# Kernel optimization log

Hardware: AMD Instinct MI355X
Metric: run time of the kernel (lower is better)

The kernel has to match this reference:

```python
import jax, jax.numpy as jnp
import numpy as np

VOCAB = 32000
EMBED = 512
NUM_CLASS = 5
LEAVES = 8192
N_NODES = 2 * LEAVES - 1


def _build_tree(n_leaves):
    """Balanced binary tree over n_leaves leaves, nodes listed in post-order
    (children always appear before their parent), matching the recursive
    traversal order of the original torch module."""
    is_leaf, word, left, right = [], [], [], []

    def rec(lo, hi):
        if hi - lo == 1:
            is_leaf.append(1)
            word.append((lo * 2654435761) % VOCAB)
            left.append(0)
            right.append(0)
        else:
            mid = (lo + hi) // 2
            l = rec(lo, mid)
            r = rec(mid, hi)
            is_leaf.append(0)
            word.append(0)
            left.append(l)
            right.append(r)
        return len(is_leaf) - 1

    rec(0, n_leaves)
    return (np.asarray(is_leaf, np.int32), np.asarray(word, np.int32),
            np.asarray(left, np.int32), np.asarray(right, np.int32))


def setup_inputs() -> dict:
    key = jax.random.key(0)
    k1, k2, k3, k4, k5 = jax.random.split(key, 5)
    is_leaf, word, left, right = _build_tree(LEAVES)
    scale = 0.05
    return {
        "is_leaf": jnp.asarray(is_leaf),
        "word": jnp.asarray(word),
        "left": jnp.asarray(left),
        "right": jnp.asarray(right),
        "emb": jax.random.normal(k1, (VOCAB, EMBED), jnp.float32) * scale,
        "W": jax.random.normal(k2, (EMBED, 2 * EMBED), jnp.float32) * scale,
        "bW": jax.random.normal(k3, (EMBED,), jnp.float32) * scale,
        "P": jax.random.normal(k4, (NUM_CLASS, EMBED), jnp.float32) * scale,
        "bP": jax.random.normal(k5, (NUM_CLASS,), jnp.float32) * scale,
    }


def reference(is_leaf, word, left, right, emb, W, bW, P, bP):
    n = is_leaf.shape[0]

    def step(H, xs):
        idx, lf, wd, li, ri = xs
        # internal node: relu(W @ [h_left; h_right] + b)
        pair = jnp.concatenate([H[li], H[ri]])          # [2D]
        internal = pair @ W.T + bW                       # [D]
        leaf = emb[wd]                                   # [D]
        h = jax.nn.relu(jnp.where(lf == 1, leaf, internal))
        return H.at[idx].set(h), None

    H0 = jnp.zeros((n, EMBED), emb.dtype)
    xs = (jnp.arange(n, dtype=jnp.int32), is_leaf, word, left, right)
    H, _ = jax.lax.scan(step, H0, xs)
    # per-node class logits, rows in traversal (post-)order: [N, num_class]
    return H @ P.T + bP
```

## Files before the change

### kernel.cpp

```cpp
#include <hip/hip_runtime.h>


#define EMBED 512
#define K2    1024
#define WOFF  (EMBED * K2)

typedef _Float16 half8 __attribute__((ext_vector_type(8)));
typedef float    floatx4 __attribute__((ext_vector_type(4)));

__device__ __forceinline__ float relu_f(float x) { return fmaxf(x, 0.0f); }

#define GLDS16(gp, lp)                                                        \
    __builtin_amdgcn_global_load_lds(                                         \
        (const __attribute__((address_space(1))) void*)(gp),                  \
        (__attribute__((address_space(3))) void*)(lp), 16, 0, 0)

__global__ __launch_bounds__(256)
void pack_w(const float* __restrict__ W,
            _Float16* __restrict__ Whp, _Float16* __restrict__ Wlp)
{
    int t = blockIdx.x * 256 + threadIdx.x;
    int n = t >> 7, kc = t & 127;
    const float* src = W + (size_t)n * K2 + kc * 8;
    int s = kc >> 2, quad = kc & 3;
    int lane = (quad << 4) | (n & 15);
    size_t off = (size_t)(n >> 4) * 16384 + (size_t)s * 512 + (size_t)lane * 8;
    half8 hi, lo;
#pragma unroll
    for (int j = 0; j < 8; ++j) {
        float w = src[j];
        _Float16 h = (_Float16)w;
        hi[j] = h;
        lo[j] = (_Float16)(w - (float)h);
    }
    *(half8*)(Whp + off) = hi;
    *(half8*)(Wlp + off) = lo;
}

__global__ __launch_bounds__(256)
void leaf_kernel(const float* __restrict__ emb, const int* __restrict__ word,
                 _Float16* __restrict__ Hh, _Float16* __restrict__ Hl, int nLeaves)
{
    int t = blockIdx.x * 256 + threadIdx.x;
    int m = t >> 6, lane = t & 63;
    if (m >= nLeaves) return;
    int idx = 2 * m - __popc(m);
    int wd = word[idx];
    const float4* src = (const float4*)(emb + (size_t)wd * EMBED) + lane * 2;
    float4 a = src[0], b = src[1];
    float v[8] = {a.x, a.y, a.z, a.w, b.x, b.y, b.z, b.w};
    half8 hi, lo;
#pragma unroll
    for (int j = 0; j < 8; ++j) {
        float x = relu_f(v[j]);
        _Float16 h = (_Float16)x;
        hi[j] = h;
        lo[j] = (_Float16)(x - (float)h);
    }
    *(half8*)(Hh + (size_t)idx * EMBED + lane * 8) = hi;
    *(half8*)(Hl + (size_t)idx * EMBED + lane * 8) = lo;
}

__global__ __launch_bounds__(256)
void gemm_big(const _Float16* H,
              const _Float16* __restrict__ Wp,
              const float* __restrict__ bW,
              _Float16* Hh, _Float16* Hl,
              int h, int M, int hoff)
{
    __shared__ _Float16 lds[48 * 512];

    int tid = threadIdx.x;
    int wave = tid >> 6, lane = tid & 63;
    int q = lane >> 4, r = lane & 15;
    int wm = wave >> 1, wn = wave & 1;
    int bm0 = blockIdx.x * 64, bn0 = blockIdx.y * 128;

    int ms = bm0 + wave * 16 + r;
    if (ms >= M) ms = M - 1;
    int node_s = ((ms + 1) << (h + 1)) - 2 - __popc(ms);
    int aL = (node_s - (1 << h)) * EMBED + q * 8;
    int aR = (node_s - 1) * EMBED + q * 8;

    floatx4 acc[2][4];
#pragma unroll
    for (int i = 0; i < 2; ++i)
#pragma unroll
        for (int j = 0; j < 4; ++j) acc[i][j] = (floatx4){0.f, 0.f, 0.f, 0.f};

    for (int kc = 0; kc < 16; ++kc) {
        int abase = (kc < 8) ? (aL + kc * 64) : (aR + (kc - 8) * 64);
#pragma unroll
        for (int i = 0; i < 4; ++i) {
            int s2 = i >> 1, hl = i & 1;
            const _Float16* gp = H + abase + s2 * 32 + (hl ? hoff : 0);
            GLDS16(gp, &lds[(wave * 4 + i) * 512]);
        }
#pragma unroll
        for (int j = 0; j < 8; ++j) {
            int u = wave * 2 + (j >> 2), s2 = (j >> 1) & 1, hl = j & 1;
            const _Float16* gp = Wp + (size_t)(blockIdx.y * 8 + u) * 16384
                               + (kc * 2 + s2) * 512 + (hl ? WOFF : 0) + lane * 8;
            GLDS16(gp, &lds[8192 + (wave * 8 + j) * 512]);
        }
        __syncthreads();

#pragma unroll
        for (int s2 = 0; s2 < 2; ++s2) {
            half8 ah[2], al[2], bh[4], bl[4];
#pragma unroll
            for (int t2 = 0; t2 < 2; ++t2) {
                int t = wm * 2 + t2;
                ah[t2] = *(const half8*)&lds[((t * 2 + s2) * 2 + 0) * 512 + lane * 8];
                al[t2] = *(const half8*)&lds[((t * 2 + s2) * 2 + 1) * 512 + lane * 8];
            }
#pragma unroll
            for (int u2 = 0; u2 < 4; ++u2) {
                int u = wn * 4 + u2;
                bh[u2] = *(const half8*)&lds[8192 + ((u * 2 + s2) * 2 + 0) * 512 + lane * 8];
                bl[u2] = *(const half8*)&lds[8192 + ((u * 2 + s2) * 2 + 1) * 512 + lane * 8];
            }
#pragma unroll
            for (int t2 = 0; t2 < 2; ++t2)
#pragma unroll
                for (int u2 = 0; u2 < 4; ++u2) {
                    acc[t2][u2] = __builtin_amdgcn_mfma_f32_16x16x32_f16(ah[t2], bh[u2], acc[t2][u2], 0, 0, 0);
                    acc[t2][u2] = __builtin_amdgcn_mfma_f32_16x16x32_f16(ah[t2], bl[u2], acc[t2][u2], 0, 0, 0);
                    acc[t2][u2] = __builtin_amdgcn_mfma_f32_16x16x32_f16(al[t2], bh[u2], acc[t2][u2], 0, 0, 0);
                }
        }
        __syncthreads();
    }

#pragma unroll
    for (int t2 = 0; t2 < 2; ++t2)
#pragma unroll
        for (int reg = 0; reg < 4; ++reg) {
            int m = bm0 + (wm * 2 + t2) * 16 + q * 4 + reg;
            if (m < M) {
                int node = ((m + 1) << (h + 1)) - 2 - __popc(m);
#pragma unroll
                for (int u2 = 0; u2 < 4; ++u2) {
                    int col = bn0 + (wn * 4 + u2) * 16 + r;
                    float v = relu_f(acc[t2][u2][reg] + bW[col]);
                    _Float16 hi = (_Float16)v;
                    Hh[(size_t)node * EMBED + col] = hi;
                    Hl[(size_t)node * EMBED + col] = (_Float16)(v - (float)hi);
                }
            }
        }
}

__global__ __launch_bounds__(256)
void gemm_splitk(const _Float16* __restrict__ Hh, const _Float16* __restrict__ Hl,
                 const _Float16* __restrict__ Wp,
                 const float* __restrict__ bW,
                 _Float16* HhO, _Float16* HlO,
                 int h, int M)
{
    __shared__ float red[4 * 256];

    int tid = threadIdx.x;
    int wave = tid >> 6, lane = tid & 63;
    int q = lane >> 4, r = lane & 15;
    int mt = blockIdx.x, u = blockIdx.y;

    int m = mt * 16 + r;
    if (m >= M) m = M - 1;
    int idx = ((m + 1) << (h + 1)) - 2 - __popc(m);
    int childRow = (wave < 2) ? (idx - (1 << h)) : (idx - 1);
    int kbase = (wave & 1) * 256;
    const _Float16* pAh = Hh + (size_t)childRow * EMBED + kbase + q * 8;
    const _Float16* pAl = Hl + (size_t)childRow * EMBED + kbase + q * 8;
    const _Float16* pB  = Wp + (size_t)u * 16384 + (size_t)(wave * 8) * 512 + lane * 8;

    floatx4 acc = (floatx4){0.f, 0.f, 0.f, 0.f};
#pragma unroll
    for (int s = 0; s < 8; ++s) {
        half8 ah = *(const half8*)(pAh + s * 32);
        half8 al = *(const half8*)(pAl + s * 32);
        half8 bh = *(const half8*)(pB + s * 512);
        half8 bl = *(const half8*)(pB + s * 512 + WOFF);
        acc = __builtin_amdgcn_mfma_f32_16x16x32_f16(ah, bh, acc, 0, 0, 0);
        acc = __builtin_amdgcn_mfma_f32_16x16x32_f16(ah, bl, acc, 0, 0, 0);
        acc = __builtin_amdgcn_mfma_f32_16x16x32_f16(al, bh, acc, 0, 0, 0);
    }
#pragma unroll
    for (int reg = 0; reg < 4; ++reg)
        red[wave * 256 + (q * 4 + reg) * 16 + r] = acc[reg];
    __syncthreads();

    int row = tid >> 4, col = tid & 15;
    float v = red[row * 16 + col] + red[256 + row * 16 + col]
            + red[512 + row * 16 + col] + red[768 + row * 16 + col];
    int mm = mt * 16 + row;
    if (mm < M) {
        int node = ((mm + 1) << (h + 1)) - 2 - __popc(mm);
        int colg = u * 16 + col;
        float x = relu_f(v + bW[colg]);
        _Float16 hi = (_Float16)x;
        HhO[(size_t)node * EMBED + colg] = hi;
        HlO[(size_t)node * EMBED + colg] = (_Float16)(x - (float)hi);
    }
}

__global__ __launch_bounds__(256)
void out_kernel(const _Float16* __restrict__ Hh, const _Float16* __restrict__ Hl,
                const float* __restrict__ P, const float* __restrict__ bP,
                float* __restrict__ out, int nNodes)
{
    int t = blockIdx.x * 256 + threadIdx.x;
    int node = t >> 6, lane = t & 63;
    if (node >= nNodes) return;
    half8 hv = *(const half8*)(Hh + (size_t)node * EMBED + lane * 8);
    half8 lv = *(const half8*)(Hl + (size_t)node * EMBED + lane * 8);
    float hx[8];
#pragma unroll
    for (int j = 0; j < 8; ++j) hx[j] = (float)hv[j] + (float)lv[j];
    float s[5];
#pragma unroll
    for (int c = 0; c < 5; ++c) {
        const float* p = P + c * EMBED + lane * 8;
        float4 p0 = *(const float4*)p;
        float4 p1 = *(const float4*)(p + 4);
        s[c] = hx[0] * p0.x + hx[1] * p0.y + hx[2] * p0.z + hx[3] * p0.w
             + hx[4] * p1.x + hx[5] * p1.y + hx[6] * p1.z + hx[7] * p1.w;
    }
#pragma unroll
    for (int o = 32; o > 0; o >>= 1)
#pragma unroll
        for (int c = 0; c < 5; ++c)
            s[c] += __shfl_down(s[c], o, 64);
    if (lane == 0) {
#pragma unroll
        for (int c = 0; c < 5; ++c)
            out[(size_t)node * 5 + c] = s[c] + bP[c];
    }
}

extern "C" void kernel_launch(void* const* d_in, const int* in_sizes, int n_in,
                              void* d_out, int out_size, void* d_ws, size_t ws_size,
                              hipStream_t stream)
{
    const int*   word = (const int*)d_in[1];
    const float* emb  = (const float*)d_in[4];
    const float* W    = (const float*)d_in[5];
    const float* bW   = (const float*)d_in[6];
    const float* P    = (const float*)d_in[7];
    const float* bP   = (const float*)d_in[8];
    float* out = (float*)d_out;

    int nNodes  = in_sizes[0];
    int nLeaves = (nNodes + 1) / 2;
    int L = 0;
    while ((1 << L) < nLeaves) ++L;

    int hoff = (nNodes + 1) * EMBED;
    _Float16* Hh  = (_Float16*)d_ws;
    _Float16* Hl  = Hh + hoff;
    _Float16* Whp = Hl + hoff;

    pack_w<<<dim3(256), dim3(256), 0, stream>>>(W, Whp, Whp + WOFF);
    leaf_kernel<<<dim3((nLeaves * 64 + 255) / 256), dim3(256), 0, stream>>>(
        emb, word, Hh, Hl, nLeaves);
    for (int h = 1; h <= L; ++h) {
        int M = 1 << (L - h);
        if (M >= 512) {
            gemm_big<<<dim3(M / 64, 4), dim3(256), 0, stream>>>(
                Hh, Whp, bW, Hh, Hl, h, M, hoff);
        } else {
            gemm_splitk<<<dim3((M + 15) / 16, 32), dim3(256), 0, stream>>>(
                Hh, Hl, Whp, bW, Hh, Hl, h, M);
        }
    }
    out_kernel<<<dim3((nNodes * 64 + 255) / 256), dim3(256), 0, stream>>>(
        Hh, Hl, P, bP, out, nNodes);
}
```

Baseline: 284.0 us.

## Fuse all tree levels into one persistent kernel with grid barriers

Replaces the sequence of per-level kernel launches (pack, leaf, 13 GEMM levels, output) with a single persistent 256-block kernel that separates the phases with atomic-counter grid barriers. The aim is to remove launch overhead and inter-kernel gaps, which are significant here because the upper tree levels carry very little work. The risks are that all 256 blocks must be co-resident for the spin barriers to make progress, that spin-waiting has its own cost, and that level count and block count are now hard-coded constants. The barrier also gives up after a spin limit instead of waiting indefinitely.

```diff
diff --git a/kernel.cpp b/kernel.cpp
--- a/kernel.cpp
+++ b/kernel.cpp
@@ -4,6 +4,8 @@
 #define EMBED 512
 #define K2    1024
 #define WOFF  (EMBED * K2)
+#define NBLK  256
+#define LVL   13
 
 typedef _Float16 half8 __attribute__((ext_vector_type(8)));
 typedef float    floatx4 __attribute__((ext_vector_type(4)));
@@ -15,226 +17,246 @@
         (const __attribute__((address_space(1))) void*)(gp),                  \
         (__attribute__((address_space(3))) void*)(lp), 16, 0, 0)
 
-__global__ __launch_bounds__(256)
-void pack_w(const float* __restrict__ W,
-            _Float16* __restrict__ Whp, _Float16* __restrict__ Wlp)
+__device__ __forceinline__ void gsync(int* cnt, int idx)
 {
-    int t = blockIdx.x * 256 + threadIdx.x;
-    int n = t >> 7, kc = t & 127;
-    const float* src = W + (size_t)n * K2 + kc * 8;
-    int s = kc >> 2, quad = kc & 3;
-    int lane = (quad << 4) | (n & 15);
-    size_t off = (size_t)(n >> 4) * 16384 + (size_t)s * 512 + (size_t)lane * 8;
-    half8 hi, lo;
-#pragma unroll
-    for (int j = 0; j < 8; ++j) {
-        float w = src[j];
-        _Float16 h = (_Float16)w;
-        hi[j] = h;
-        lo[j] = (_Float16)(w - (float)h);
-    }
-    *(half8*)(Whp + off) = hi;
-    *(half8*)(Wlp + off) = lo;
+    __syncthreads();
+    if (threadIdx.x == 0) {
+        __threadfence();
+        __hip_atomic_fetch_add(&cnt[idx], 1, __ATOMIC_RELEASE,
+                               __HIP_MEMORY_SCOPE_AGENT);
+        int spins = 0;
+        while (__hip_atomic_load(&cnt[idx], __ATOMIC_ACQUIRE,
+                                 __HIP_MEMORY_SCOPE_AGENT) < NBLK) {
+            __builtin_amdgcn_s_sleep(2);
+            if (++spins > (1 << 22)) break;
+        }
+        __threadfence();
+    }
+    __syncthreads();
 }
 
-__global__ __launch_bounds__(256)
-void leaf_kernel(const float* __restrict__ emb, const int* __restrict__ word,
-                 _Float16* __restrict__ Hh, _Float16* __restrict__ Hl, int nLeaves)
-{
-    int t = blockIdx.x * 256 + threadIdx.x;
-    int m = t >> 6, lane = t & 63;
-    if (m >= nLeaves) return;
-    int idx = 2 * m - __popc(m);
-    int wd = word[idx];
-    const float4* src = (const float4*)(emb + (size_t)wd * EMBED) + lane * 2;
-    float4 a = src[0], b = src[1];
-    float v[8] = {a.x, a.y, a.z, a.w, b.x, b.y, b.z, b.w};
-    half8 hi, lo;
-#pragma unroll
-    for (int j = 0; j < 8; ++j) {
-        float x = relu_f(v[j]);
-        _Float16 h = (_Float16)x;
-        hi[j] = h;
-        lo[j] = (_Float16)(x - (float)h);
-    }
-    *(half8*)(Hh + (size_t)idx * EMBED + lane * 8) = hi;
-    *(half8*)(Hl + (size_t)idx * EMBED + lane * 8) = lo;
-}
-
-__global__ __launch_bounds__(256)
-void gemm_big(const _Float16* H,
-              const _Float16* __restrict__ Wp,
-              const float* __restrict__ bW,
-              _Float16* Hh, _Float16* Hl,
-              int h, int M, int hoff)
+__global__ __launch_bounds__(256, 1)
+void mega(const int* __restrict__ word, const float* __restrict__ emb,
+          const float* __restrict__ W, const float* __restrict__ bW,
+          const float* __restrict__ P, const float* __restrict__ bP,
+          _Float16* Hh, _Float16* Hl,
+          _Float16* Whp,
+          int* cnt, float* out, int nNodes, int nLeaves, int hoff)
 {
     __shared__ _Float16 lds[48 * 512];
+    float* red = (float*)lds;
 
     int tid = threadIdx.x;
     int wave = tid >> 6, lane = tid & 63;
     int q = lane >> 4, r = lane & 15;
     int wm = wave >> 1, wn = wave & 1;
-    int bm0 = blockIdx.x * 64, bn0 = blockIdx.y * 128;
-
-    int ms = bm0 + wave * 16 + r;
-    if (ms >= M) ms = M - 1;
-    int node_s = ((ms + 1) << (h + 1)) - 2 - __popc(ms);
-    int aL = (node_s - (1 << h)) * EMBED + q * 8;
-    int aR = (node_s - 1) * EMBED + q * 8;
-
-    floatx4 acc[2][4];
-#pragma unroll
-    for (int i = 0; i < 2; ++i)
-#pragma unroll
-        for (int j = 0; j < 4; ++j) acc[i][j] = (floatx4){0.f, 0.f, 0.f, 0.f};
-
-    for (int kc = 0; kc < 16; ++kc) {
-        int abase = (kc < 8) ? (aL + kc * 64) : (aR + (kc - 8) * 64);
-#pragma unroll
-        for (int i = 0; i < 4; ++i) {
-            int s2 = i >> 1, hl = i & 1;
-            const _Float16* gp = H + abase + s2 * 32 + (hl ? hoff : 0);
-            GLDS16(gp, &lds[(wave * 4 + i) * 512]);
-        }
+
+    {
+        int t = blockIdx.x * 256 + tid;
+        int n = t >> 7, kc = t & 127;
+        const float* src = W + (size_t)n * K2 + kc * 8;
+        int s = kc >> 2, quad = kc & 3;
+        int ln = (quad << 4) | (n & 15);
+        size_t off = (size_t)(n >> 4) * 16384 + (size_t)s * 512 + (size_t)ln * 8;
+        half8 hi, lo;
 #pragma unroll
         for (int j = 0; j < 8; ++j) {
-            int u = wave * 2 + (j >> 2), s2 = (j >> 1) & 1, hl = j & 1;
-            const _Float16* gp = Wp + (size_t)(blockIdx.y * 8 + u) * 16384
-                               + (kc * 2 + s2) * 512 + (hl ? WOFF : 0) + lane * 8;
-            GLDS16(gp, &lds[8192 + (wave * 8 + j) * 512]);
-        }
-        __syncthreads();
-
-#pragma unroll
-        for (int s2 = 0; s2 < 2; ++s2) {
-            half8 ah[2], al[2], bh[4], bl[4];
-#pragma unroll
-            for (int t2 = 0; t2 < 2; ++t2) {
-                int t = wm * 2 + t2;
-                ah[t2] = *(const half8*)&lds[((t * 2 + s2) * 2 + 0) * 512 + lane * 8];
-                al[t2] = *(const half8*)&lds[((t * 2 + s2) * 2 + 1) * 512 + lane * 8];
-            }
-#pragma unroll
-            for (int u2 = 0; u2 < 4; ++u2) {
-                int u = wn * 4 + u2;
-                bh[u2] = *(const half8*)&lds[8192 + ((u * 2 + s2) * 2 + 0) * 512 + lane * 8];
-                bl[u2] = *(const half8*)&lds[8192 + ((u * 2 + s2) * 2 + 1) * 512 + lane * 8];
-            }
+            float w = src[j];
+            _Float16 h16 = (_Float16)w;
+            hi[j] = h16;
+            lo[j] = (_Float16)(w - (float)h16);
+        }
+        *(half8*)(Whp + off) = hi;
+        *(half8*)(Whp + WOFF + off) = lo;
+    }
+    {
+#pragma unroll
+        for (int i = 0; i < 8; ++i) {
+            int m = blockIdx.x * 32 + wave * 8 + i;
+            if (m < nLeaves) {
+                int idx = 2 * m - __popc(m);
+                int wd = word[idx];
+                const float4* src = (const float4*)(emb + (size_t)wd * EMBED) + lane * 2;
+                float4 a = src[0], b = src[1];
+                float v[8] = {a.x, a.y, a.z, a.w, b.x, b.y, b.z, b.w};
+                half8 hi, lo;
+#pragma unroll
+                for (int j = 0; j < 8; ++j) {
+                    float x = relu_f(v[j]);
+                    _Float16 h16 = (_Float16)x;
+                    hi[j] = h16;
+                    lo[j] = (_Float16)(x - (float)h16);
+                }
+                *(half8*)(Hh + (size_t)idx * EMBED + lane * 8) = hi;
+                *(half8*)(Hl + (size_t)idx * EMBED + lane * 8) = lo;
+            }
+        }
+    }
+    gsync(cnt, 0);
+
+    for (int h = 1; h <= 4; ++h) {
+        int M = 1 << (LVL - h);
+        int mtiles = M >> 6;
+        int jobs = mtiles * 4;
+        if ((int)blockIdx.x < jobs) {
+            int bx = blockIdx.x % mtiles, by = blockIdx.x / mtiles;
+            int bm0 = bx * 64, bn0 = by * 128;
+
+            int ms = bm0 + wave * 16 + r;
+            if (ms >= M) ms = M - 1;
+            int node_s = ((ms + 1) << (h + 1)) - 2 - __popc(ms);
+            int aL = (node_s - (1 << h)) * EMBED + q * 8;
+            int aR = (node_s - 1) * EMBED + q * 8;
+
+            floatx4 acc[2][4];
+#pragma unroll
+            for (int i = 0; i < 2; ++i)
+#pragma unroll
+                for (int j = 0; j < 4; ++j) acc[i][j] = (floatx4){0.f, 0.f, 0.f, 0.f};
+
+            for (int kc = 0; kc < 16; ++kc) {
+                int abase = (kc < 8) ? (aL + kc * 64) : (aR + (kc - 8) * 64);
+#pragma unroll
+                for (int i = 0; i < 4; ++i) {
+                    int s2 = i >> 1, hl = i & 1;
+                    const _Float16* gp = Hh + abase + s2 * 32 + (hl ? hoff : 0);
+                    GLDS16(gp, &lds[(wave * 4 + i) * 512]);
+                }
+#pragma unroll
+                for (int j = 0; j < 8; ++j) {
+                    int u = wave * 2 + (j >> 2), s2 = (j >> 1) & 1, hl = j & 1;
+                    const _Float16* gp = Whp + (size_t)(by * 8 + u) * 16384
+                                       + (kc * 2 + s2) * 512 + (hl ? WOFF : 0) + lane * 8;
+                    GLDS16(gp, &lds[8192 + (wave * 8 + j) * 512]);
+                }
+                __syncthreads();
+
+#pragma unroll
+                for (int s2 = 0; s2 < 2; ++s2) {
+                    half8 ah[2], al[2], bh[4], bl[4];
+#pragma unroll
+                    for (int t2 = 0; t2 < 2; ++t2) {
+                        int t = wm * 2 + t2;
+                        ah[t2] = *(const half8*)&lds[((t * 2 + s2) * 2 + 0) * 512 + lane * 8];
+                        al[t2] = *(const half8*)&lds[((t * 2 + s2) * 2 + 1) * 512 + lane * 8];
+                    }
+#pragma unroll
+                    for (int u2 = 0; u2 < 4; ++u2) {
+                        int u = wn * 4 + u2;
+                        bh[u2] = *(const half8*)&lds[8192 + ((u * 2 + s2) * 2 + 0) * 512 + lane * 8];
+                        bl[u2] = *(const half8*)&lds[8192 + ((u * 2 + s2) * 2 + 1) * 512 + lane * 8];
+                    }
+#pragma unroll
+                    for (int t2 = 0; t2 < 2; ++t2)
+#pragma unroll
+                        for (int u2 = 0; u2 < 4; ++u2) {
+                            acc[t2][u2] = __builtin_amdgcn_mfma_f32_16x16x32_f16(ah[t2], bh[u2], acc[t2][u2], 0, 0, 0);
+                            acc[t2][u2] = __builtin_amdgcn_mfma_f32_16x16x32_f16(ah[t2], bl[u2], acc[t2][u2], 0, 0, 0);
+                            acc[t2][u2] = __builtin_amdgcn_mfma_f32_16x16x32_f16(al[t2], bh[u2], acc[t2][u2], 0, 0, 0);
+                        }
+                }
+                __syncthreads();
+            }
+
 #pragma unroll
             for (int t2 = 0; t2 < 2; ++t2)
 #pragma unroll
-                for (int u2 = 0; u2 < 4; ++u2) {
-                    acc[t2][u2] = __builtin_amdgcn_mfma_f32_16x16x32_f16(ah[t2], bh[u2], acc[t2][u2], 0, 0, 0);
-                    acc[t2][u2] = __builtin_amdgcn_mfma_f32_16x16x32_f16(ah[t2], bl[u2], acc[t2][u2], 0, 0, 0);
-                    acc[t2][u2] = __builtin_amdgcn_mfma_f32_16x16x32_f16(al[t2], bh[u2], acc[t2][u2], 0, 0, 0);
-                }
-        }
-        __syncthreads();
-    }
-
-#pragma unroll
-    for (int t2 = 0; t2 < 2; ++t2)
-#pragma unroll
-        for (int reg = 0; reg < 4; ++reg) {
-            int m = bm0 + (wm * 2 + t2) * 16 + q * 4 + reg;
-            if (m < M) {
-                int node = ((m + 1) << (h + 1)) - 2 - __popc(m);
-#pragma unroll
-                for (int u2 = 0; u2 < 4; ++u2) {
-                    int col = bn0 + (wn * 4 + u2) * 16 + r;
-                    float v = relu_f(acc[t2][u2][reg] + bW[col]);
-                    _Float16 hi = (_Float16)v;
-                    Hh[(size_t)node * EMBED + col] = hi;
-                    Hl[(size_t)node * EMBED + col] = (_Float16)(v - (float)hi);
-                }
-            }
-        }
-}
-
-__global__ __launch_bounds__(256)
-void gemm_splitk(const _Float16* __restrict__ Hh, const _Float16* __restrict__ Hl,
-                 const _Float16* __restrict__ Wp,
-                 const float* __restrict__ bW,
-                 _Float16* HhO, _Float16* HlO,
-                 int h, int M)
-{
-    __shared__ float red[4 * 256];
-
-    int tid = threadIdx.x;
-    int wave = tid >> 6, lane = tid & 63;
-    int q = lane >> 4, r = lane & 15;
-    int mt = blockIdx.x, u = blockIdx.y;
-
-    int m = mt * 16 + r;
-    if (m >= M) m = M - 1;
-    int idx = ((m + 1) << (h + 1)) - 2 - __popc(m);
-    int childRow = (wave < 2) ? (idx - (1 << h)) : (idx - 1);
-    int kbase = (wave & 1) * 256;
-    const _Float16* pAh = Hh + (size_t)childRow * EMBED + kbase + q * 8;
-    const _Float16* pAl = Hl + (size_t)childRow * EMBED + kbase + q * 8;
-    const _Float16* pB  = Wp + (size_t)u * 16384 + (size_t)(wave * 8) * 512 + lane * 8;
-
-    floatx4 acc = (floatx4){0.f, 0.f, 0.f, 0.f};
-#pragma unroll
-    for (int s = 0; s < 8; ++s) {
-        half8 ah = *(const half8*)(pAh + s * 32);
-        half8 al = *(const half8*)(pAl + s * 32);
-        half8 bh = *(const half8*)(pB + s * 512);
-        half8 bl = *(const half8*)(pB + s * 512 + WOFF);
-        acc = __builtin_amdgcn_mfma_f32_16x16x32_f16(ah, bh, acc, 0, 0, 0);
-        acc = __builtin_amdgcn_mfma_f32_16x16x32_f16(ah, bl, acc, 0, 0, 0);
-        acc = __builtin_amdgcn_mfma_f32_16x16x32_f16(al, bh, acc, 0, 0, 0);
-    }
-#pragma unroll
-    for (int reg = 0; reg < 4; ++reg)
-        red[wave * 256 + (q * 4 + reg) * 16 + r] = acc[reg];
-    __syncthreads();
-
-    int row = tid >> 4, col = tid & 15;
-    float v = red[row * 16 + col] + red[256 + row * 16 + col]
-            + red[512 + row * 16 + col] + red[768 + row * 16 + col];
-    int mm = mt * 16 + row;
-    if (mm < M) {
-        int node = ((mm + 1) << (h + 1)) - 2 - __popc(mm);
-        int colg = u * 16 + col;
-        float x = relu_f(v + bW[colg]);
-        _Float16 hi = (_Float16)x;
-        HhO[(size_t)node * EMBED + colg] = hi;
-        HlO[(size_t)node * EMBED + colg] = (_Float16)(x - (float)hi);
-    }
-}
-
-__global__ __launch_bounds__(256)
-void out_kernel(const _Float16* __restrict__ Hh, const _Float16* __restrict__ Hl,
-                const float* __restrict__ P, const float* __restrict__ bP,
-                float* __restrict__ out, int nNodes)
-{
-    int t = blockIdx.x * 256 + threadIdx.x;
-    int node = t >> 6, lane = t & 63;
-    if (node >= nNodes) return;
-    half8 hv = *(const half8*)(Hh + (size_t)node * EMBED + lane * 8);
-    half8 lv = *(const half8*)(Hl + (size_t)node * EMBED + lane * 8);
-    float hx[8];
-#pragma unroll
-    for (int j = 0; j < 8; ++j) hx[j] = (float)hv[j] + (float)lv[j];
-    float s[5];
-#pragma unroll
-    for (int c = 0; c < 5; ++c) {
-        const float* p = P + c * EMBED + lane * 8;
-        float4 p0 = *(const float4*)p;
-        float4 p1 = *(const float4*)(p + 4);
-        s[c] = hx[0] * p0.x + hx[1] * p0.y + hx[2] * p0.z + hx[3] * p0.w
-             + hx[4] * p1.x + hx[5] * p1.y + hx[6] * p1.z + hx[7] * p1.w;
-    }
-#pragma unroll
-    for (int o = 32; o > 0; o >>= 1)
-#pragma unroll
-        for (int c = 0; c < 5; ++c)
-            s[c] += __shfl_down(s[c], o, 64);
-    if (lane == 0) {
-#pragma unroll
-        for (int c = 0; c < 5; ++c)
-            out[(size_t)node * 5 + c] = s[c] + bP[c];
+                for (int reg = 0; reg < 4; ++reg) {
+                    int m = bm0 + (wm * 2 + t2) * 16 + q * 4 + reg;
+                    if (m < M) {
+                        int node = ((m + 1) << (h + 1)) - 2 - __popc(m);
+#pragma unroll
+                        for (int u2 = 0; u2 < 4; ++u2) {
+                            int col = bn0 + (wn * 4 + u2) * 16 + r;
+                            float v = relu_f(acc[t2][u2][reg] + bW[col]);
+                            _Float16 hi = (_Float16)v;
+                            Hh[(size_t)node * EMBED + col] = hi;
+                            Hl[(size_t)node * EMBED + col] = (_Float16)(v - (float)hi);
+                        }
+                    }
+                }
+        }
+        gsync(cnt, h);
+    }
+
+    for (int h = 5; h <= LVL; ++h) {
+        int M = 1 << (LVL - h);
+        int jm = (M + 15) >> 4;
+        int jobs = jm * 32;
+        for (int job = blockIdx.x; job < jobs; job += NBLK) {
+            int mt = job % jm, u = job / jm;
+
+            int m = mt * 16 + r;
+            if (m >= M) m = M - 1;
+            int idx = ((m + 1) << (h + 1)) - 2 - __popc(m);
+            int childRow = (wave < 2) ? (idx - (1 << h)) : (idx - 1);
+            int kbase = (wave & 1) * 256;
+            const _Float16* pAh = Hh + (size_t)childRow * EMBED + kbase + q * 8;
+            const _Float16* pAl = Hl + (size_t)childRow * EMBED + kbase + q * 8;
+            const _Float16* pB  = Whp + (size_t)u * 16384 + (size_t)(wave * 8) * 512 + lane * 8;
+
+            floatx4 acc = (floatx4){0.f, 0.f, 0.f, 0.f};
+#pragma unroll
+            for (int s = 0; s < 8; ++s) {
+                half8 ah = *(const half8*)(pAh + s * 32);
+                half8 al = *(const half8*)(pAl + s * 32);
+                half8 bh = *(const half8*)(pB + s * 512);
+                half8 bl = *(const half8*)(pB + s * 512 + WOFF);
+                acc = __builtin_amdgcn_mfma_f32_16x16x32_f16(ah, bh, acc, 0, 0, 0);
+                acc = __builtin_amdgcn_mfma_f32_16x16x32_f16(ah, bl, acc, 0, 0, 0);
+                acc = __builtin_amdgcn_mfma_f32_16x16x32_f16(al, bh, acc, 0, 0, 0);
+            }
+#pragma unroll
+            for (int reg = 0; reg < 4; ++reg)
+                red[wave * 256 + (q * 4 + reg) * 16 + r] = acc[reg];
+            __syncthreads();
+
+            int row = tid >> 4, col = tid & 15;
+            float v = red[row * 16 + col] + red[256 + row * 16 + col]
+                    + red[512 + row * 16 + col] + red[768 + row * 16 + col];
+            int mm = mt * 16 + row;
+            if (mm < M) {
+                int node = ((mm + 1) << (h + 1)) - 2 - __popc(mm);
+                int colg = u * 16 + col;
+                float x = relu_f(v + bW[colg]);
+                _Float16 hi = (_Float16)x;
+                Hh[(size_t)node * EMBED + colg] = hi;
+                Hl[(size_t)node * EMBED + colg] = (_Float16)(x - (float)hi);
+            }
+            __syncthreads();
+        }
+        gsync(cnt, h);
+    }
+
+#pragma unroll
+    for (int i = 0; i < 16; ++i) {
+        int node = blockIdx.x * 64 + wave * 16 + i;
+        if (node < nNodes) {
+            half8 hv = *(const half8*)(Hh + (size_t)node * EMBED + lane * 8);
+            half8 lv = *(const half8*)(Hl + (size_t)node * EMBED + lane * 8);
+            float hx[8];
+#pragma unroll
+            for (int j = 0; j < 8; ++j) hx[j] = (float)hv[j] + (float)lv[j];
+            float s[5];
+#pragma unroll
+            for (int c = 0; c < 5; ++c) {
+                const float* p = P + c * EMBED + lane * 8;
+                float4 p0 = *(const float4*)p;
+                float4 p1 = *(const float4*)(p + 4);
+                s[c] = hx[0] * p0.x + hx[1] * p0.y + hx[2] * p0.z + hx[3] * p0.w
+                     + hx[4] * p1.x + hx[5] * p1.y + hx[6] * p1.z + hx[7] * p1.w;
+            }
+#pragma unroll
+            for (int o = 32; o > 0; o >>= 1)
+#pragma unroll
+                for (int c = 0; c < 5; ++c)
+                    s[c] += __shfl_down(s[c], o, 64);
+            if (lane == 0) {
+#pragma unroll
+                for (int c = 0; c < 5; ++c)
+                    out[(size_t)node * 5 + c] = s[c] + bP[c];
+            }
+        }
     }
 }
 
@@ -252,27 +274,14 @@
 
     int nNodes  = in_sizes[0];
     int nLeaves = (nNodes + 1) / 2;
-    int L = 0;
-    while ((1 << L) < nLeaves) ++L;
 
     int hoff = (nNodes + 1) * EMBED;
     _Float16* Hh  = (_Float16*)d_ws;
     _Float16* Hl  = Hh + hoff;
     _Float16* Whp = Hl + hoff;
-
-    pack_w<<<dim3(256), dim3(256), 0, stream>>>(W, Whp, Whp + WOFF);
-    leaf_kernel<<<dim3((nLeaves * 64 + 255) / 256), dim3(256), 0, stream>>>(
-        emb, word, Hh, Hl, nLeaves);
-    for (int h = 1; h <= L; ++h) {
-        int M = 1 << (L - h);
-        if (M >= 512) {
-            gemm_big<<<dim3(M / 64, 4), dim3(256), 0, stream>>>(
-                Hh, Whp, bW, Hh, Hl, h, M, hoff);
-        } else {
-            gemm_splitk<<<dim3((M + 15) / 16, 32), dim3(256), 0, stream>>>(
-                Hh, Hl, Whp, bW, Hh, Hl, h, M);
-        }
-    }
-    out_kernel<<<dim3((nNodes * 64 + 255) / 256), dim3(256), 0, stream>>>(
-        Hh, Hl, P, bP, out, nNodes);
+    int* cnt = (int*)(Whp + 2 * WOFF);
+
+    hipMemsetAsync(cnt, 0, 64, stream);
+    mega<<<dim3(NBLK), dim3(256), 0, stream>>>(
+        word, emb, W, bW, P, bP, Hh, Hl, Whp, cnt, out, nNodes, nLeaves, hoff);
 }
```

After: 830.3 us. 2.92x slower.

## Fuse small tree levels into persistent tail kernel with atomic job queues

Applied to the files above, without the earlier changes.

Replaces the per-level split-K launches for the small upper tree levels with one persistent kernel. Blocks pull jobs from atomic counters grouped by XCC id and spin-wait on a completion counter between levels. It also merges W packing and leaf embedding into one kernel and doubles the K-chunk staged per iteration in gemm_big. The aim is to remove launch overhead and tail latency for the many tiny levels, at the cost of inter-block spin synchronization, which depends on all blocks being co-resident and on per-XCC L2 visibility. The tree depth is hard-coded for 8192 leaves.

```diff
diff --git a/kernel.cpp b/kernel.cpp
--- a/kernel.cpp
+++ b/kernel.cpp
@@ -16,59 +16,68 @@
         (__attribute__((address_space(3))) void*)(lp), 16, 0, 0)
 
 __global__ __launch_bounds__(256)
-void pack_w(const float* __restrict__ W,
-            _Float16* __restrict__ Whp, _Float16* __restrict__ Wlp)
-{
-    int t = blockIdx.x * 256 + threadIdx.x;
-    int n = t >> 7, kc = t & 127;
-    const float* src = W + (size_t)n * K2 + kc * 8;
-    int s = kc >> 2, quad = kc & 3;
-    int lane = (quad << 4) | (n & 15);
-    size_t off = (size_t)(n >> 4) * 16384 + (size_t)s * 512 + (size_t)lane * 8;
-    half8 hi, lo;
-#pragma unroll
-    for (int j = 0; j < 8; ++j) {
-        float w = src[j];
-        _Float16 h = (_Float16)w;
-        hi[j] = h;
-        lo[j] = (_Float16)(w - (float)h);
-    }
-    *(half8*)(Whp + off) = hi;
-    *(half8*)(Wlp + off) = lo;
-}
-
-__global__ __launch_bounds__(256)
-void leaf_kernel(const float* __restrict__ emb, const int* __restrict__ word,
-                 _Float16* __restrict__ Hh, _Float16* __restrict__ Hl, int nLeaves)
-{
-    int t = blockIdx.x * 256 + threadIdx.x;
-    int m = t >> 6, lane = t & 63;
-    if (m >= nLeaves) return;
-    int idx = 2 * m - __popc(m);
-    int wd = word[idx];
-    const float4* src = (const float4*)(emb + (size_t)wd * EMBED) + lane * 2;
-    float4 a = src[0], b = src[1];
-    float v[8] = {a.x, a.y, a.z, a.w, b.x, b.y, b.z, b.w};
-    half8 hi, lo;
-#pragma unroll
-    for (int j = 0; j < 8; ++j) {
-        float x = relu_f(v[j]);
-        _Float16 h = (_Float16)x;
-        hi[j] = h;
-        lo[j] = (_Float16)(x - (float)h);
-    }
-    *(half8*)(Hh + (size_t)idx * EMBED + lane * 8) = hi;
-    *(half8*)(Hl + (size_t)idx * EMBED + lane * 8) = lo;
-}
-
-__global__ __launch_bounds__(256)
+void packleaf(const float* __restrict__ W, const float* __restrict__ emb,
+              const int* __restrict__ word,
+              _Float16* __restrict__ Whp,
+              _Float16* __restrict__ Hh, _Float16* __restrict__ Hl,
+              int* __restrict__ cnt, int nLeaves)
+{
+    int tid = threadIdx.x;
+    int wave = tid >> 6, lane = tid & 63;
+
+    if (blockIdx.x == 0) cnt[tid] = 0;
+
+    {
+        int t = blockIdx.x * 256 + tid;
+        int n = t >> 7, kc = t & 127;
+        const float* src = W + (size_t)n * K2 + kc * 8;
+        int s = kc >> 2, quad = kc & 3;
+        int ln = (quad << 4) | (n & 15);
+        size_t off = (size_t)(n >> 4) * 16384 + (size_t)s * 512 + (size_t)ln * 8;
+        half8 hi, lo;
+#pragma unroll
+        for (int j = 0; j < 8; ++j) {
+            float w = src[j];
+            _Float16 h16 = (_Float16)w;
+            hi[j] = h16;
+            lo[j] = (_Float16)(w - (float)h16);
+        }
+        *(half8*)(Whp + off) = hi;
+        *(half8*)(Whp + WOFF + off) = lo;
+    }
+    {
+#pragma unroll
+        for (int i = 0; i < 8; ++i) {
+            int m = blockIdx.x * 32 + wave * 8 + i;
+            if (m < nLeaves) {
+                int idx = 2 * m - __popc(m);
+                int wd = word[idx];
+                const float4* src = (const float4*)(emb + (size_t)wd * EMBED) + lane * 2;
+                float4 a = src[0], b = src[1];
+                float v[8] = {a.x, a.y, a.z, a.w, b.x, b.y, b.z, b.w};
+                half8 hi, lo;
+#pragma unroll
+                for (int j = 0; j < 8; ++j) {
+                    float x = relu_f(v[j]);
+                    _Float16 h16 = (_Float16)x;
+                    hi[j] = h16;
+                    lo[j] = (_Float16)(x - (float)h16);
+                }
+                *(half8*)(Hh + (size_t)idx * EMBED + lane * 8) = hi;
+                *(half8*)(Hl + (size_t)idx * EMBED + lane * 8) = lo;
+            }
+        }
+    }
+}
+
+__global__ __launch_bounds__(256, 1)
 void gemm_big(const _Float16* H,
               const _Float16* __restrict__ Wp,
               const float* __restrict__ bW,
               _Float16* Hh, _Float16* Hl,
               int h, int M, int hoff)
 {
-    __shared__ _Float16 lds[48 * 512];
+    __shared__ _Float16 lds[49152];
 
     int tid = threadIdx.x;
     int wave = tid >> 6, lane = tid & 63;
@@ -88,37 +97,37 @@
 #pragma unroll
         for (int j = 0; j < 4; ++j) acc[i][j] = (floatx4){0.f, 0.f, 0.f, 0.f};
 
-    for (int kc = 0; kc < 16; ++kc) {
-        int abase = (kc < 8) ? (aL + kc * 64) : (aR + (kc - 8) * 64);
-#pragma unroll
-        for (int i = 0; i < 4; ++i) {
+    for (int kc = 0; kc < 8; ++kc) {
+        int abase = ((kc < 4) ? aL : aR) + (kc & 3) * 128;
+#pragma unroll
+        for (int i = 0; i < 8; ++i) {
             int s2 = i >> 1, hl = i & 1;
             const _Float16* gp = H + abase + s2 * 32 + (hl ? hoff : 0);
-            GLDS16(gp, &lds[(wave * 4 + i) * 512]);
-        }
-#pragma unroll
-        for (int j = 0; j < 8; ++j) {
-            int u = wave * 2 + (j >> 2), s2 = (j >> 1) & 1, hl = j & 1;
+            GLDS16(gp, &lds[(wave * 8 + i) * 512]);
+        }
+#pragma unroll
+        for (int j = 0; j < 16; ++j) {
+            int u = wave * 2 + (j >> 3), s2 = (j >> 1) & 3, hl = j & 1;
             const _Float16* gp = Wp + (size_t)(blockIdx.y * 8 + u) * 16384
-                               + (kc * 2 + s2) * 512 + (hl ? WOFF : 0) + lane * 8;
-            GLDS16(gp, &lds[8192 + (wave * 8 + j) * 512]);
+                               + (kc * 4 + s2) * 512 + (hl ? WOFF : 0) + lane * 8;
+            GLDS16(gp, &lds[16384 + (wave * 16 + j) * 512]);
         }
         __syncthreads();
 
 #pragma unroll
-        for (int s2 = 0; s2 < 2; ++s2) {
+        for (int s2 = 0; s2 < 4; ++s2) {
             half8 ah[2], al[2], bh[4], bl[4];
 #pragma unroll
             for (int t2 = 0; t2 < 2; ++t2) {
                 int t = wm * 2 + t2;
-                ah[t2] = *(const half8*)&lds[((t * 2 + s2) * 2 + 0) * 512 + lane * 8];
-                al[t2] = *(const half8*)&lds[((t * 2 + s2) * 2 + 1) * 512 + lane * 8];
+                ah[t2] = *(const half8*)&lds[(t * 8 + s2 * 2 + 0) * 512 + lane * 8];
+                al[t2] = *(const half8*)&lds[(t * 8 + s2 * 2 + 1) * 512 + lane * 8];
             }
 #pragma unroll
             for (int u2 = 0; u2 < 4; ++u2) {
                 int u = wn * 4 + u2;
-                bh[u2] = *(const half8*)&lds[8192 + ((u * 2 + s2) * 2 + 0) * 512 + lane * 8];
-                bl[u2] = *(const half8*)&lds[8192 + ((u * 2 + s2) * 2 + 1) * 512 + lane * 8];
+                bh[u2] = *(const half8*)&lds[16384 + (u * 8 + s2 * 2 + 0) * 512 + lane * 8];
+                bl[u2] = *(const half8*)&lds[16384 + (u * 8 + s2 * 2 + 1) * 512 + lane * 8];
             }
 #pragma unroll
             for (int t2 = 0; t2 < 2; ++t2)
@@ -152,55 +161,79 @@
 }
 
 __global__ __launch_bounds__(256)
-void gemm_splitk(const _Float16* __restrict__ Hh, const _Float16* __restrict__ Hl,
-                 const _Float16* __restrict__ Wp,
-                 const float* __restrict__ bW,
-                 _Float16* HhO, _Float16* HlO,
-                 int h, int M)
-{
-    __shared__ float red[4 * 256];
-
+void tail(_Float16* Hh, _Float16* Hl,
+          const _Float16* __restrict__ Wp,
+          const float* __restrict__ bW,
+          int* __restrict__ cnt)
+{
+    __shared__ int sjob;
     int tid = threadIdx.x;
     int wave = tid >> 6, lane = tid & 63;
     int q = lane >> 4, r = lane & 15;
-    int mt = blockIdx.x, u = blockIdx.y;
-
-    int m = mt * 16 + r;
-    if (m >= M) m = M - 1;
-    int idx = ((m + 1) << (h + 1)) - 2 - __popc(m);
-    int childRow = (wave < 2) ? (idx - (1 << h)) : (idx - 1);
-    int kbase = (wave & 1) * 256;
-    const _Float16* pAh = Hh + (size_t)childRow * EMBED + kbase + q * 8;
-    const _Float16* pAl = Hl + (size_t)childRow * EMBED + kbase + q * 8;
-    const _Float16* pB  = Wp + (size_t)u * 16384 + (size_t)(wave * 8) * 512 + lane * 8;
-
-    floatx4 acc = (floatx4){0.f, 0.f, 0.f, 0.f};
-#pragma unroll
-    for (int s = 0; s < 8; ++s) {
-        half8 ah = *(const half8*)(pAh + s * 32);
-        half8 al = *(const half8*)(pAl + s * 32);
-        half8 bh = *(const half8*)(pB + s * 512);
-        half8 bl = *(const half8*)(pB + s * 512 + WOFF);
-        acc = __builtin_amdgcn_mfma_f32_16x16x32_f16(ah, bh, acc, 0, 0, 0);
-        acc = __builtin_amdgcn_mfma_f32_16x16x32_f16(ah, bl, acc, 0, 0, 0);
-        acc = __builtin_amdgcn_mfma_f32_16x16x32_f16(al, bh, acc, 0, 0, 0);
-    }
-#pragma unroll
-    for (int reg = 0; reg < 4; ++reg)
-        red[wave * 256 + (q * 4 + reg) * 16 + r] = acc[reg];
-    __syncthreads();
-
-    int row = tid >> 4, col = tid & 15;
-    float v = red[row * 16 + col] + red[256 + row * 16 + col]
-            + red[512 + row * 16 + col] + red[768 + row * 16 + col];
-    int mm = mt * 16 + row;
-    if (mm < M) {
-        int node = ((mm + 1) << (h + 1)) - 2 - __popc(mm);
-        int colg = u * 16 + col;
-        float x = relu_f(v + bW[colg]);
-        _Float16 hi = (_Float16)x;
-        HhO[(size_t)node * EMBED + colg] = hi;
-        HlO[(size_t)node * EMBED + colg] = (_Float16)(x - (float)hi);
+
+    int g = (int)__builtin_amdgcn_s_getreg((31 << 11) | 20) & 7;
+
+    for (int h = 5; h <= 13; ++h) {
+        int lM = 13 - h;
+        int M = 1 << lM;
+        int lmt = (lM > 4) ? (lM - 4) : 0;
+        int jobs = (1 << lmt) * 8;
+        int* pc = &cnt[g * 32 + (h - 5)];
+        int* pd = &cnt[g * 32 + 16 + (h - 5)];
+
+        for (;;) {
+            if (tid == 0) sjob = atomicAdd(pc, 1);
+            __syncthreads();
+            int job = sjob;
+            if (job >= jobs) { __syncthreads(); break; }
+
+            int s = job & ((1 << lmt) - 1);
+            int c = job >> lmt;
+            int m = s * 16 + r;
+            if (m >= M) m = M - 1;
+            int idx = ((m + 1) << (h + 1)) - 2 - __popc(m);
+            const _Float16* pLh = Hh + (size_t)(idx - (1 << h)) * EMBED + q * 8;
+            const _Float16* pLl = Hl + (size_t)(idx - (1 << h)) * EMBED + q * 8;
+            const _Float16* pRh = Hh + (size_t)(idx - 1) * EMBED + q * 8;
+            const _Float16* pRl = Hl + (size_t)(idx - 1) * EMBED + q * 8;
+            const _Float16* pB  = Wp + (size_t)(c * 4 + wave) * 16384 + lane * 8;
+
+            floatx4 acc = (floatx4){0.f, 0.f, 0.f, 0.f};
+#pragma unroll 8
+            for (int k = 0; k < 32; ++k) {
+                half8 ah = *(const half8*)((k < 16) ? (pLh + k * 32) : (pRh + (k - 16) * 32));
+                half8 al = *(const half8*)((k < 16) ? (pLl + k * 32) : (pRl + (k - 16) * 32));
+                half8 bh = *(const half8*)(pB + k * 512);
+                half8 bl = *(const half8*)(pB + k * 512 + WOFF);
+                acc = __builtin_amdgcn_mfma_f32_16x16x32_f16(ah, bh, acc, 0, 0, 0);
+                acc = __builtin_amdgcn_mfma_f32_16x16x32_f16(ah, bl, acc, 0, 0, 0);
+                acc = __builtin_amdgcn_mfma_f32_16x16x32_f16(al, bh, acc, 0, 0, 0);
+            }
+            int colg = (c * 4 + wave) * 16 + r;
+            float bw = bW[colg];
+#pragma unroll
+            for (int reg = 0; reg < 4; ++reg) {
+                int mm = s * 16 + q * 4 + reg;
+                if (mm < M) {
+                    int node = ((mm + 1) << (h + 1)) - 2 - __popc(mm);
+                    float v = relu_f(acc[reg] + bw);
+                    _Float16 hi = (_Float16)v;
+                    Hh[(size_t)node * EMBED + colg] = hi;
+                    Hl[(size_t)node * EMBED + colg] = (_Float16)(v - (float)hi);
+                }
+            }
+            __syncthreads();
+            if (tid == 0) atomicAdd(pd, 1);
+        }
+
+        if (tid == 0) {
+            int spins = 0;
+            while (atomicAdd(pd, 0) < jobs) {
+                __builtin_amdgcn_s_sleep(2);
+                if (++spins > (1 << 24)) break;
+            }
+        }
+        __syncthreads();
     }
 }
 
@@ -252,27 +285,21 @@
 
     int nNodes  = in_sizes[0];
     int nLeaves = (nNodes + 1) / 2;
-    int L = 0;
-    while ((1 << L) < nLeaves) ++L;
 
     int hoff = (nNodes + 1) * EMBED;
     _Float16* Hh  = (_Float16*)d_ws;
     _Float16* Hl  = Hh + hoff;
     _Float16* Whp = Hl + hoff;
-
-    pack_w<<<dim3(256), dim3(256), 0, stream>>>(W, Whp, Whp + WOFF);
-    leaf_kernel<<<dim3((nLeaves * 64 + 255) / 256), dim3(256), 0, stream>>>(
-        emb, word, Hh, Hl, nLeaves);
-    for (int h = 1; h <= L; ++h) {
-        int M = 1 << (L - h);
-        if (M >= 512) {
-            gemm_big<<<dim3(M / 64, 4), dim3(256), 0, stream>>>(
-                Hh, Whp, bW, Hh, Hl, h, M, hoff);
-        } else {
-            gemm_splitk<<<dim3((M + 15) / 16, 32), dim3(256), 0, stream>>>(
-                Hh, Hl, Whp, bW, Hh, Hl, h, M);
-        }
-    }
+    int* cnt = (int*)(Whp + 2 * WOFF);
+
+    packleaf<<<dim3(256), dim3(256), 0, stream>>>(
+        W, emb, word, Whp, Hh, Hl, cnt, nLeaves);
+    for (int h = 1; h <= 4; ++h) {
+        int M = 1 << (13 - h);
+        gemm_big<<<dim3(M / 64, 4), dim3(256), 0, stream>>>(
+            Hh, Whp, bW, Hh, Hl, h, M, hoff);
+    }
+    tail<<<dim3(256), dim3(256), 0, stream>>>(Hh, Hl, Whp, bW, cnt);
     out_kernel<<<dim3((nNodes * 64 + 255) / 256), dim3(256), 0, stream>>>(
         Hh, Hl, P, bP, out, nNodes);
 }
```

After: 409.6 us. 44.2% more time.
